# Performance work log

Measured on AMD Instinct MI355X. Metric: run time of the kernel, lower is better.

Reference implementation:

```python
import jax, jax.numpy as jnp
import numpy as np

RATIOS = (0.5, 1.0, 2.0)
SCALES = (8.0, 16.0, 32.0)
NUM_LANDMARKS = 6   # NMS max_output_size
IOU_THRESH = 0.5    # tf.image.non_max_suppression default


def _generate_anchors(fh, fw, ih, iw):
    # stride of backbone in each dim
    x_stride = iw / fw
    y_stride = ih / fh
    xs = (jnp.arange(fw, dtype=jnp.float32) + 0.5) * x_stride
    ys = (jnp.arange(fh, dtype=jnp.float32) + 0.5) * y_stride
    cy, cx = jnp.meshgrid(ys, xs, indexing='ij')              # [fh, fw]
    # 9 anchor (h, w) pairs: ratio-major, scale-minor
    h = jnp.array([np.sqrt(s * s / r) * y_stride for r in RATIOS for s in SCALES], jnp.float32)
    w = h * jnp.array([r for r in RATIOS for _ in SCALES], jnp.float32) * (x_stride / y_stride)
    cx = cx[..., None]
    cy = cy[..., None]
    anchors = jnp.stack([cx - w / 2, cy - h / 2, cx + w / 2, cy + h / 2], axis=-1)  # [fh,fw,9,4]
    anchors = anchors.reshape(-1, 4)                                               # [N,4]
    valid = (anchors[:, 0] >= 0) & (anchors[:, 1] >= 0) & \
            (anchors[:, 2] <= iw) & (anchors[:, 3] <= ih)
    return anchors, valid


def _conv(x, w, b):
    y = jax.lax.conv_general_dilated(x, w, (1, 1), 'SAME',
                                     dimension_numbers=('NHWC', 'HWIO', 'NHWC'))
    return y + b


def _iou_one_vs_all(box, boxes):
    x1 = jnp.maximum(box[0], boxes[:, 0])
    y1 = jnp.maximum(box[1], boxes[:, 1])
    x2 = jnp.minimum(box[2], boxes[:, 2])
    y2 = jnp.minimum(box[3], boxes[:, 3])
    inter = jnp.maximum(x2 - x1, 0.0) * jnp.maximum(y2 - y1, 0.0)
    a1 = (box[2] - box[0]) * (box[3] - box[1])
    a2 = (boxes[:, 2] - boxes[:, 0]) * (boxes[:, 3] - boxes[:, 1])
    return inter / (a1 + a2 - inter + 1e-9)


def setup_inputs() -> dict:
    key = jax.random.key(0)
    ks = jax.random.split(key, 8)
    STD = 0.05  # keras RandomNormal default stddev
    return {
        'features': jax.random.normal(ks[0], (1, 160, 160, 512), jnp.float32),
        'image':    jnp.zeros((1, 2560, 2560, 3), jnp.float32),  # only shape is consumed
        'conv1_w':  jax.random.normal(ks[1], (3, 3, 512, 512), jnp.float32) * STD,
        'conv1_b':  jnp.zeros((512,), jnp.float32),
        'reg_w':    jax.random.normal(ks[2], (1, 1, 512, 72), jnp.float32) * STD,
        'reg_b':    jnp.zeros((72,), jnp.float32),
        'cls_w':    jax.random.normal(ks[3], (1, 1, 512, 9), jnp.float32) * STD,
        'cls_b':    jnp.zeros((9,), jnp.float32),
        'lm_w':     jax.random.normal(ks[4], (1, 1, 512, 54), jnp.float32) * STD,
        'lm_b':     jnp.zeros((54,), jnp.float32),
    }


def reference(features, image, conv1_w, conv1_b, reg_w, reg_b, cls_w, cls_b, lm_w, lm_b):
    fh, fw = features.shape[1], features.shape[2]
    ih, iw = float(image.shape[1]), float(image.shape[2])
    anchors, valid = _generate_anchors(fh, fw, ih, iw)        # [N,4], [N]

    x = jax.nn.relu(_conv(features, conv1_w, conv1_b))        # [1,fh,fw,512]
    deltas = _conv(x, reg_w, reg_b).reshape(-1, 8)[:, :4]     # [N,4] (dx,dy,dw,dh)
    scores = jax.nn.sigmoid(_conv(x, cls_w, cls_b)).reshape(-1)  # [N]
    eye_landmarks = _conv(x, lm_w, lm_b)                      # [1,fh,fw,54]

    # decode anchor deltas -> corner boxes, clipped to the image
    wa = anchors[:, 2] - anchors[:, 0]
    ha = anchors[:, 3] - anchors[:, 1]
    xa = anchors[:, 0] + wa / 2
    ya = anchors[:, 1] + ha / 2
    px = xa + wa * deltas[:, 0]
    py = ya + ha * deltas[:, 1]
    pw = wa * jnp.exp(deltas[:, 2])
    ph = ha * jnp.exp(deltas[:, 3])
    x1 = px - pw / 2
    y1 = py - ph / 2
    boxes = jnp.stack([jnp.clip(x1, 0, iw), jnp.clip(y1, 0, ih),
                       jnp.clip(x1 + pw, 0, iw), jnp.clip(y1 + ph, 0, ih)], axis=-1)

    # greedy NMS, fixed 6 outputs (out-of-image anchors masked out)
    def body(k, carry):
        sel, alive = carry
        s = jnp.where(alive & valid, scores, -1.0)
        i = jnp.argmax(s).astype(jnp.int32)
        iou = _iou_one_vs_all(boxes[i], boxes)
        alive = alive & (iou <= IOU_THRESH)
        return sel.at[k].set(i), alive

    sel, _ = jax.lax.fori_loop(
        0, NUM_LANDMARKS, body,
        (jnp.zeros((NUM_LANDMARKS,), jnp.int32), jnp.ones((boxes.shape[0],), bool)))
    rois = boxes[sel]                                         # [6,4]
    return rois, eye_landmarks, anchors
```

## Files before the change

kernel.cpp:

```cpp
#include <hip/hip_runtime.h>
#include <math.h>

#define FH 160
#define FW 160
#define NPOS (FH*FW)
#define NANCH (NPOS*9)
#define IMG 2560.0f
#define STRIDE 16.0f

typedef __attribute__((ext_vector_type(8))) _Float16 half8;
typedef __attribute__((ext_vector_type(4))) float f32x4;
typedef unsigned long long u64;

__device__ __forceinline__ unsigned short f2h(float v) {
    _Float16 h = (_Float16)v;
    return *(unsigned short*)&h;
}
__device__ __forceinline__ void g2l16(void* lds, const void* g) {
    __builtin_amdgcn_global_load_lds(
        (const __attribute__((address_space(1))) void*)g,
        (__attribute__((address_space(3))) void*)lds, 16, 0, 0);
}
__device__ __forceinline__ u64 pack_key(float s, int n) {
    unsigned int bu = __float_as_uint(s);
    unsigned int key = (bu & 0x80000000u) ? ~bu : (bu | 0x80000000u);
    return ((u64)key << 32) | (unsigned int)~(unsigned int)n;
}
__device__ __forceinline__ u64 wave_max64(u64 v) {
#pragma unroll
    for (int off = 32; off > 0; off >>= 1) {
        u64 o = __shfl_xor(v, off, 64);
        v = v > o ? v : o;
    }
    return v;
}

__global__ __launch_bounds__(256) void prep_kernel(
    const float* __restrict__ f, const float* __restrict__ w,
    const float* __restrict__ regw, const float* __restrict__ clsw,
    const float* __restrict__ lmw,
    unsigned short* __restrict__ fph, unsigned short* __restrict__ wt,
    unsigned short* __restrict__ wh)
{
    __shared__ float tile[32][33];
    const int bid = blockIdx.x, t = threadIdx.x;
    if (bid < 13122) {
        int idx = bid*256 + t;
        int c4 = (idx & 127) << 2;
        int rest = idx >> 7;
        int x = rest % 162, y = rest / 162;
        float4 v = make_float4(0.f, 0.f, 0.f, 0.f);
        if (y > 0 && y < 161 && x > 0 && x < 161)
            v = *(const float4*)(f + ((size_t)((y-1)*FW + (x-1)) << 9) + c4);
        ushort4 h;
        h.x = f2h(v.x); h.y = f2h(v.y); h.z = f2h(v.z); h.w = f2h(v.w);
        *(ushort4*)(fph + ((size_t)(y*162 + x) << 9) + c4) = h;
    } else if (bid < 15426) {
        int b = bid - 13122;
        int k0 = (b % 144)*32, oc0 = (b / 144)*32;
        int c = t & 31, r8 = t >> 5;
#pragma unroll
        for (int i = 0; i < 4; ++i) {
            int r = r8 + i*8;
            tile[c][r] = w[(size_t)(k0 + r)*512 + oc0 + c];
        }
        __syncthreads();
#pragma unroll
        for (int i = 0; i < 4; ++i) {
            int orow = r8 + i*8, kcol = c;
            wt[(size_t)(oc0 + orow)*4608 + k0 + kcol] = f2h(tile[orow][kcol]);
        }
    } else {
        int i = (bid - 15426)*256 + t;
        int u = i >> 9, c = i & 511;
        float v = 0.f;
        if (u < 36)      v = regw[c*72 + (u>>2)*8 + (u&3)];
        else if (u < 45) v = clsw[c*9 + (u-36)];
        else if (u < 99) v = lmw[c*54 + (u-45)];
        wh[i] = f2h(v);
    }
}

__global__ __launch_bounds__(256) void conv1_mfma_kernel(
    const unsigned short* __restrict__ fph, const unsigned short* __restrict__ wt,
    const float* __restrict__ bias, unsigned short* __restrict__ xh)
{
    __shared__ unsigned short As[128*64];
    __shared__ unsigned short Bs[128*64];
    const int tid  = threadIdx.x;
    const int lane = tid & 63;
    const int wi   = (tid >> 7) & 1;
    const int wj   = (tid >> 6) & 1;
    const int bid  = blockIdx.x;
    const int xcd  = bid & 7, sl = bid >> 3;
    const int oc0  = (xcd & 3) * 128;
    const int pt   = (xcd >> 2) * 100 + sl;
    const int ty = pt / 5, tx = pt - ty*5;
    const int y0 = ty*4, x0 = tx*32;

    const int srow = tid >> 3;
    const int kswz = (((tid & 7) ^ (srow & 7)) << 3);
    const int quad = lane >> 4, fr = lane & 15;

    f32x4 acc[4][4] = {};
    const size_t bBase = (size_t)(oc0 + srow)*4608 + kswz;

    for (int tap = 0; tap < 9; ++tap) {
        const int ky = tap/3, kx = tap - (tap/3)*3;
        const size_t aBase = ((size_t)((y0 + ky)*162 + (x0 + srow + kx)) << 9) + kswz;
        const size_t bTap  = bBase + tap*512;
        for (int icb = 0; icb < 512; icb += 64) {
#pragma unroll
            for (int r = 0; r < 4; ++r) {
                g2l16(As + tid*8 + r*2048, fph + aBase + (size_t)r*162*512 + icb);
                g2l16(Bs + tid*8 + r*2048, wt  + bTap  + (size_t)r*32*4608 + icb);
            }
            __syncthreads();
#pragma unroll
            for (int kk = 0; kk < 2; ++kk) {
                const int sa = ((kk*4 + quad) ^ (fr & 7)) << 3;
                half8 a[4], b[4];
#pragma unroll
                for (int i = 0; i < 4; ++i) {
                    a[i] = *(const half8*)(As + (wi*64 + i*16 + fr)*64 + sa);
                    b[i] = *(const half8*)(Bs + (wj*64 + i*16 + fr)*64 + sa);
                }
#pragma unroll
                for (int i = 0; i < 4; ++i)
#pragma unroll
                    for (int j = 0; j < 4; ++j)
                        acc[i][j] = __builtin_amdgcn_mfma_f32_16x16x32_f16(a[i], b[j], acc[i][j], 0, 0, 0);
            }
            __syncthreads();
        }
    }

#pragma unroll
    for (int i = 0; i < 4; ++i) {
#pragma unroll
        for (int r = 0; r < 4; ++r) {
            int mi = wi*64 + i*16 + quad*4 + r;
            int p = (y0 + (mi >> 5))*FW + x0 + (mi & 31);
#pragma unroll
            for (int j = 0; j < 4; ++j) {
                int col = oc0 + wj*64 + j*16 + fr;
                float v = acc[i][j][r] + bias[col];
                xh[(size_t)p*512 + col] = f2h(v > 0.f ? v : 0.f);
            }
        }
    }
}

__global__ __launch_bounds__(256) void heads_mfma_kernel(
    const unsigned short* __restrict__ xh, const unsigned short* __restrict__ wh,
    const float* __restrict__ regb, const float* __restrict__ clsb,
    const float* __restrict__ lmb,
    float* __restrict__ lm_out, float* __restrict__ boxes,
    float* __restrict__ anch_out, float* __restrict__ s_arr,
    u64* __restrict__ blockmax)
{
    __shared__ union SM {
        struct { unsigned short As[128*64]; unsigned short Bs[128*64]; } g;
        struct { float sdel[128][40]; float scls[128][12]; u64 red[8]; } e;
    } sm;
    unsigned short* As = sm.g.As;
    unsigned short* Bs = sm.g.Bs;
    const int tid  = threadIdx.x;
    const int lane = tid & 63;
    const int wi   = (tid >> 7) & 1;
    const int wj   = (tid >> 6) & 1;
    const int p0   = blockIdx.x * 128;

    const int srow = tid >> 3;
    const int kswz = (((tid & 7) ^ (srow & 7)) << 3);
    const int quad = lane >> 4, fr = lane & 15;
    f32x4 acc[4][4] = {};

    const size_t aOfs = ((size_t)(p0 + srow) << 9) + kswz;
    const size_t bOfs = ((size_t)srow << 9) + kswz;

    for (int icb = 0; icb < 512; icb += 64) {
#pragma unroll
        for (int r = 0; r < 4; ++r) {
            g2l16(As + tid*8 + r*2048, xh + aOfs + (size_t)r*32*512 + icb);
            g2l16(Bs + tid*8 + r*2048, wh + bOfs + (size_t)r*32*512 + icb);
        }
        __syncthreads();
#pragma unroll
        for (int kk = 0; kk < 2; ++kk) {
            const int sa = ((kk*4 + quad) ^ (fr & 7)) << 3;
            half8 a[4], b[4];
#pragma unroll
            for (int i = 0; i < 4; ++i) {
                a[i] = *(const half8*)(As + (wi*64 + i*16 + fr)*64 + sa);
                b[i] = *(const half8*)(Bs + (wj*64 + i*16 + fr)*64 + sa);
            }
#pragma unroll
            for (int i = 0; i < 4; ++i)
#pragma unroll
                for (int j = 0; j < 4; ++j)
                    acc[i][j] = __builtin_amdgcn_mfma_f32_16x16x32_f16(a[i], b[j], acc[i][j], 0, 0, 0);
        }
        __syncthreads();
    }

#pragma unroll
    for (int i = 0; i < 4; ++i) {
#pragma unroll
        for (int r = 0; r < 4; ++r) {
            int pl = wi*64 + i*16 + quad*4 + r;
            int p = p0 + pl;
#pragma unroll
            for (int j = 0; j < 4; ++j) {
                int u = wj*64 + j*16 + fr;
                float v = acc[i][j][r];
                if (u < 36) {
                    sm.e.sdel[pl][u] = v + regb[(u>>2)*8 + (u&3)];
                } else if (u < 45) {
                    float z = v + clsb[u-36];
                    sm.e.scls[pl][u-36] = 1.f/(1.f + expf(-z));
                } else if (u < 99) {
                    lm_out[(size_t)p*54 + (u-45)] = v + lmb[u-45];
                }
            }
        }
    }
    __syncthreads();

    u64 local = 0ull;
    for (int t = tid; t < 128*9; t += 256) {
        int pl = t / 9, a = t - pl*9;
        int p = p0 + pl;
        int y = p / FW, x = p - FW*y;
        float cx = (x + 0.5f)*STRIDE, cy = (y + 0.5f)*STRIDE;
        const float rr[3] = {0.5f, 1.f, 2.f};
        const float ss[3] = {8.f, 16.f, 32.f};
        float r = rr[a/3], sv = ss[a - (a/3)*3];
        float h  = sqrtf(sv*sv/r)*STRIDE;
        float wvv = h * r;
        float x1a = cx - wvv*0.5f, y1a = cy - h*0.5f;
        float x2a = cx + wvv*0.5f, y2a = cy + h*0.5f;
        size_t n = (size_t)p*9 + a;
        float4 av = {x1a, y1a, x2a, y2a};
        *(float4*)(anch_out + 4*n) = av;
        bool valid = (x1a >= 0.f) && (y1a >= 0.f) && (x2a <= IMG) && (y2a <= IMG);

        float dx = sm.e.sdel[pl][a*4+0], dy = sm.e.sdel[pl][a*4+1];
        float dw = sm.e.sdel[pl][a*4+2], dh = sm.e.sdel[pl][a*4+3];
        float px = cx + wvv*dx, py = cy + h*dy;
        float pw = wvv*expf(dw), ph = h*expf(dh);
        float bx1 = px - pw*0.5f, by1 = py - ph*0.5f;
        float4 b;
        b.x = fminf(fmaxf(bx1, 0.f), IMG);
        b.y = fminf(fmaxf(by1, 0.f), IMG);
        b.z = fminf(fmaxf(bx1 + pw, 0.f), IMG);
        b.w = fminf(fmaxf(by1 + ph, 0.f), IMG);
        *(float4*)(boxes + 4*n) = b;
        float s = valid ? sm.e.scls[pl][a] : -1.f;
        s_arr[n] = s;
        u64 pk = pack_key(s, (int)n);
        local = local > pk ? local : pk;
    }
    local = wave_max64(local);
    if ((tid & 63) == 0) sm.e.red[tid >> 6] = local;
    __syncthreads();
    if (tid == 0) {
        u64 m = sm.e.red[0];
        m = m > sm.e.red[1] ? m : sm.e.red[1];
        m = m > sm.e.red[2] ? m : sm.e.red[2];
        m = m > sm.e.red[3] ? m : sm.e.red[3];
        blockmax[blockIdx.x] = m;
    }
}

__global__ __launch_bounds__(256) void nms_supp_kernel(
    const float* __restrict__ boxes, float* __restrict__ s_arr,
    u64* __restrict__ blockmax, float* __restrict__ rois, int k)
{
    __shared__ u64 red[4];
    __shared__ u64 win_sh;
    const int tid = threadIdx.x;

    u64 v = (tid < 200) ? blockmax[tid] : 0ull;
    v = wave_max64(v);
    if ((tid & 63) == 0) red[tid >> 6] = v;
    __syncthreads();
    if (tid == 0) {
        u64 m = red[0];
        m = m > red[1] ? m : red[1];
        m = m > red[2] ? m : red[2];
        m = m > red[3] ? m : red[3];
        win_sh = m;
    }
    __syncthreads();
    const unsigned int wn = ~(unsigned int)(win_sh & 0xFFFFFFFFull);
    const float4 wb = *(const float4*)(boxes + (size_t)4*wn);
    if (blockIdx.x == 0 && tid == 0)
        *(float4*)(rois + 4*(k-1)) = wb;

    const float wa = (wb.z - wb.x)*(wb.w - wb.y);
    const int base = blockIdx.x * 1152;
    u64 local = 0ull;
    for (int i = tid; i < 1152; i += 256) {
        int n = base + i;
        float s = s_arr[n];
        float4 b = *(const float4*)(boxes + (size_t)4*n);
        float ix = fminf(wb.z, b.z) - fmaxf(wb.x, b.x);
        float iy = fminf(wb.w, b.w) - fmaxf(wb.y, b.y);
        float inter = fmaxf(ix, 0.f)*fmaxf(iy, 0.f);
        float a2 = (b.z - b.x)*(b.w - b.y);
        float iou = inter/(wa + a2 - inter + 1e-9f);
        if (iou > 0.5f && s > -1.f) { s = -1.f; s_arr[n] = -1.f; }
        u64 pk = pack_key(s, n);
        local = local > pk ? local : pk;
    }
    local = wave_max64(local);
    if ((tid & 63) == 0) red[tid >> 6] = local;
    __syncthreads();
    if (tid == 0) {
        u64 m = red[0];
        m = m > red[1] ? m : red[1];
        m = m > red[2] ? m : red[2];
        m = m > red[3] ? m : red[3];
        blockmax[blockIdx.x] = m;
    }
}

__global__ void nms_fin2_kernel(
    const float* __restrict__ boxes, const u64* __restrict__ blockmax,
    float* __restrict__ rois)
{
    __shared__ u64 red[4];
    const int tid = threadIdx.x;
    u64 v = (tid < 200) ? blockmax[tid] : 0ull;
    v = wave_max64(v);
    if ((tid & 63) == 0) red[tid >> 6] = v;
    __syncthreads();
    if (tid == 0) {
        u64 m = red[0];
        m = m > red[1] ? m : red[1];
        m = m > red[2] ? m : red[2];
        m = m > red[3] ? m : red[3];
        unsigned int wn = ~(unsigned int)(m & 0xFFFFFFFFull);
        *(float4*)(rois + 20) = *(const float4*)(boxes + (size_t)4*wn);
    }
}

__global__ __launch_bounds__(256) void conv1_kernel(
    const float* __restrict__ f, const float* __restrict__ w,
    const float* __restrict__ bias, float* __restrict__ xout)
{
    __shared__ float As2[32][66];
    __shared__ float Bs2[32][66];
    const int tid = threadIdx.x;
    const int nt = blockIdx.x;
    const int mt = blockIdx.y;
    const int p0 = mt*64, oc0 = nt*64;
    const int tm = tid & 15, tn = tid >> 4;
    const int kA = tid & 31, mA = tid >> 5;
    const int nB = tid & 63, kB = tid >> 6;
    int yv[8], xv[8];
#pragma unroll
    for (int it = 0; it < 8; ++it) {
        int p = p0 + mA + it*8;
        yv[it] = p / FW;
        xv[it] = p - yv[it]*FW;
    }
    float acc[4][4] = {};
    for (int tap = 0; tap < 9; ++tap) {
        const int ky = tap/3 - 1, kx = tap%3 - 1;
        for (int icb = 0; icb < 512; icb += 32) {
#pragma unroll
            for (int it = 0; it < 8; ++it) {
                int yy = yv[it] + ky, xx = xv[it] + kx;
                float v = 0.f;
                if ((unsigned)yy < (unsigned)FH && (unsigned)xx < (unsigned)FW)
                    v = f[(((yy*FW)+xx)<<9) + icb + kA];
                As2[kA][mA + it*8] = v;
            }
            const float* wp = w + ((size_t)(tap*512 + icb + kB))*512 + oc0 + nB;
#pragma unroll
            for (int it = 0; it < 8; ++it)
                Bs2[kB + it*4][nB] = wp[(size_t)it*4*512];
            __syncthreads();
#pragma unroll 8
            for (int kk = 0; kk < 32; ++kk) {
                float a0 = As2[kk][4*tm+0], a1 = As2[kk][4*tm+1],
                      a2 = As2[kk][4*tm+2], a3 = As2[kk][4*tm+3];
                float b0 = Bs2[kk][4*tn+0], b1 = Bs2[kk][4*tn+1],
                      b2 = Bs2[kk][4*tn+2], b3 = Bs2[kk][4*tn+3];
                acc[0][0] += a0*b0; acc[0][1] += a0*b1; acc[0][2] += a0*b2; acc[0][3] += a0*b3;
                acc[1][0] += a1*b0; acc[1][1] += a1*b1; acc[1][2] += a1*b2; acc[1][3] += a1*b3;
                acc[2][0] += a2*b0; acc[2][1] += a2*b1; acc[2][2] += a2*b2; acc[2][3] += a2*b3;
                acc[3][0] += a3*b0; acc[3][1] += a3*b1; acc[3][2] += a3*b2; acc[3][3] += a3*b3;
            }
            __syncthreads();
        }
    }
#pragma unroll
    for (int i = 0; i < 4; ++i) {
        int p = p0 + 4*tm + i;
        float4 o;
        float* op = &o.x;
#pragma unroll
        for (int j = 0; j < 4; ++j) {
            float v = acc[i][j] + bias[oc0 + 4*tn + j];
            op[j] = v > 0.f ? v : 0.f;
        }
        *(float4*)(xout + (size_t)p*512 + oc0 + 4*tn) = o;
    }
}

__global__ __launch_bounds__(256) void wprep_kernel(
    const float* __restrict__ regw, const float* __restrict__ clsw,
    const float* __restrict__ lmw, float* __restrict__ wT)
{
    int i = blockIdx.x*256 + threadIdx.x;
    if (i >= 99*512) return;
    int u = i >> 9, c = i & 511;
    float v;
    if (u < 36)      v = regw[c*72 + (u>>2)*8 + (u&3)];
    else if (u < 45) v = clsw[c*9 + (u-36)];
    else             v = lmw[c*54 + (u-45)];
    wT[i] = v;
}

__global__ __launch_bounds__(256) void heads_kernel(
    const float* __restrict__ x, const float* __restrict__ wT,
    const float* __restrict__ regb, const float* __restrict__ clsb,
    const float* __restrict__ lmb,
    float* __restrict__ lm_out, float* __restrict__ deltas,
    float* __restrict__ s_arr)
{
    __shared__ float xs[16*516];
    const int p0 = blockIdx.x * 16;
    const float4* src = (const float4*)(x + (size_t)p0*512);
    for (int i = threadIdx.x; i < 16*128; i += 256) {
        int row = i >> 7, c4 = i & 127;
        *(float4*)(xs + row*516 + c4*4) = src[row*128 + c4];
    }
    __syncthreads();
    for (int oi = threadIdx.x; oi < 99*16; oi += 256) {
        int ps = oi & 15, u = oi >> 4;
        const float4* wv = (const float4*)(wT + (u << 9));
        const float4* xv = (const float4*)(xs + ps*516);
        float acc = 0.f;
#pragma unroll 4
        for (int c = 0; c < 128; ++c) {
            float4 a = xv[c], b = wv[c];
            acc += a.x*b.x + a.y*b.y + a.z*b.z + a.w*b.w;
        }
        int p = p0 + ps;
        if (u < 36) {
            int aidx = u >> 2, r = u & 3;
            deltas[(size_t)(p*9 + aidx)*4 + r] = acc + regb[aidx*8 + r];
        } else if (u < 45) {
            float z = acc + clsb[u-36];
            s_arr[p*9 + (u-36)] = 1.f/(1.f + expf(-z));
        } else {
            lm_out[(size_t)p*54 + (u-45)] = acc + lmb[u-45];
        }
    }
}

__global__ __launch_bounds__(256) void decode_kernel(
    const float* __restrict__ deltas, float* __restrict__ s_arr,
    float* __restrict__ boxes, float* __restrict__ anch_out,
    u64* __restrict__ slot)
{
    int n = blockIdx.x*256 + threadIdx.x;
    if (n < 8) slot[n] = 0ull;
    if (n >= NANCH) return;
    int p = n / 9, a = n - 9*p;
    int y = p / FW, x = p - FW*y;
    float cx = (x + 0.5f)*STRIDE, cy = (y + 0.5f)*STRIDE;
    const float rr[3] = {0.5f, 1.f, 2.f};
    const float ss[3] = {8.f, 16.f, 32.f};
    float r = rr[a/3], sv = ss[a - (a/3)*3];
    float h  = sqrtf(sv*sv/r)*STRIDE;
    float wv = h * r;
    float x1a = cx - wv*0.5f, y1a = cy - h*0.5f;
    float x2a = cx + wv*0.5f, y2a = cy + h*0.5f;
    float4 av = {x1a, y1a, x2a, y2a};
    *(float4*)(anch_out + (size_t)4*n) = av;
    bool valid = (x1a >= 0.f) && (y1a >= 0.f) && (x2a <= IMG) && (y2a <= IMG);

    float4 d = *(const float4*)(deltas + (size_t)4*n);
    float px = cx + wv*d.x, py = cy + h*d.y;
    float pw = wv*expf(d.z), ph = h*expf(d.w);
    float bx1 = px - pw*0.5f, by1 = py - ph*0.5f;
    float4 b;
    b.x = fminf(fmaxf(bx1, 0.f), IMG);
    b.y = fminf(fmaxf(by1, 0.f), IMG);
    b.z = fminf(fmaxf(bx1 + pw, 0.f), IMG);
    b.w = fminf(fmaxf(by1 + ph, 0.f), IMG);
    *(float4*)(boxes + (size_t)4*n) = b;
    if (!valid) s_arr[n] = -1.f;
}

__global__ __launch_bounds__(256) void nms_iter_kernel(
    const float* __restrict__ boxes, float* __restrict__ s_arr,
    u64* __restrict__ slot, int k)
{
    __shared__ u64 red[4];
    int n = blockIdx.x*256 + threadIdx.x;
    float s = s_arr[n];
    if (k > 0) {
        unsigned int wn = ~(unsigned int)(slot[k-1] & 0xFFFFFFFFull);
        float4 wb = *(const float4*)(boxes + (size_t)4*wn);
        float4 b  = *(const float4*)(boxes + (size_t)4*n);
        float ix = fminf(wb.z, b.z) - fmaxf(wb.x, b.x);
        float iy = fminf(wb.w, b.w) - fmaxf(wb.y, b.y);
        float inter = fmaxf(ix, 0.f)*fmaxf(iy, 0.f);
        float a1 = (wb.z-wb.x)*(wb.w-wb.y);
        float a2 = (b.z-b.x)*(b.w-b.y);
        float iou = inter/(a1 + a2 - inter + 1e-9f);
        if (iou > 0.5f) { s = -1.f; s_arr[n] = -1.f; }
    }
    u64 packed = pack_key(s, n);
    packed = wave_max64(packed);
    if ((threadIdx.x & 63) == 0) red[threadIdx.x >> 6] = packed;
    __syncthreads();
    if (threadIdx.x == 0) {
        u64 m = red[0];
        m = m > red[1] ? m : red[1];
        m = m > red[2] ? m : red[2];
        m = m > red[3] ? m : red[3];
        atomicMax(&slot[k], m);
    }
}

__global__ void nms_fin_kernel(
    const float* __restrict__ boxes,
    const u64* __restrict__ slot, float* __restrict__ rois)
{
    int t = threadIdx.x;
    if (t < 6) {
        unsigned int n = ~(unsigned int)(slot[t] & 0xFFFFFFFFull);
        float4 b = *(const float4*)(boxes + (size_t)4*n);
        *(float4*)(rois + 4*t) = b;
    }
}

extern "C" void kernel_launch(void* const* d_in, const int* in_sizes, int n_in,
                              void* d_out, int out_size, void* d_ws, size_t ws_size,
                              hipStream_t stream)
{
    const float* f    = (const float*)d_in[0];
    const float* c1w  = (const float*)d_in[2];
    const float* c1b  = (const float*)d_in[3];
    const float* regw = (const float*)d_in[4];
    const float* regb = (const float*)d_in[5];
    const float* clsw = (const float*)d_in[6];
    const float* clsb = (const float*)d_in[7];
    const float* lmw  = (const float*)d_in[8];
    const float* lmb  = (const float*)d_in[9];

    float* out      = (float*)d_out;
    float* rois     = out;
    float* lm_out   = out + 24;
    float* anch_out = out + 24 + (size_t)NPOS*54;

    char* ws = (char*)d_ws;

    if (ws_size >= 62547968ull) {
        u64* blockmax = (u64*)ws;
        unsigned short* wh  = (unsigned short*)(ws + 2048);
        unsigned short* fph = (unsigned short*)(ws + 133120);
        unsigned short* wt  = (unsigned short*)(ws + 27006976);
        unsigned short* xh  = (unsigned short*)(ws + 31725568);
        float* boxes  = (float*)(ws + 57939968);
        float* s_arr  = (float*)(ws + 61626368);

        prep_kernel<<<15682, 256, 0, stream>>>(f, c1w, regw, clsw, lmw,
                                               fph, wt, wh);
        conv1_mfma_kernel<<<800, 256, 0, stream>>>(fph, wt, c1b, xh);
        heads_mfma_kernel<<<200, 256, 0, stream>>>(xh, wh, regb, clsb, lmb,
                                                   lm_out, boxes, anch_out,
                                                   s_arr, blockmax);
        for (int k = 1; k <= 5; ++k)
            nms_supp_kernel<<<200, 256, 0, stream>>>(boxes, s_arr, blockmax,
                                                     rois, k);
        nms_fin2_kernel<<<1, 256, 0, stream>>>(boxes, blockmax, rois);
    } else {
        u64* slot = (u64*)ws;
        float* wT     = (float*)(ws + 256);
        float* boxes  = (float*)(ws + 256 + 202752);
        float* deltas = (float*)(ws + 256 + 202752 + 3686400);
        float* s_arr  = (float*)(ws + 256 + 202752 + 2*3686400);
        float* x      = (float*)(ws + 256 + 202752 + 2*3686400 + 921600);

        wprep_kernel<<<(99*512 + 255)/256, 256, 0, stream>>>(regw, clsw, lmw, wT);
        conv1_kernel<<<dim3(8, 400), 256, 0, stream>>>(f, c1w, c1b, x);
        heads_kernel<<<NPOS/16, 256, 0, stream>>>(x, wT, regb, clsb, lmb,
                                                  lm_out, deltas, s_arr);
        decode_kernel<<<NANCH/256, 256, 0, stream>>>(deltas, s_arr, boxes,
                                                     anch_out, slot);
        for (int k = 0; k < 6; ++k)
            nms_iter_kernel<<<NANCH/256, 256, 0, stream>>>(boxes, s_arr, slot, k);
        nms_fin_kernel<<<1, 64, 0, stream>>>(boxes, slot, rois);
    }
}
```

Measured before the change: 388.5 us.

## Fuse NMS iterations into heads kernel via grid-wide barrier

```diff
diff --git a/kernel.cpp b/kernel.cpp
--- a/kernel.cpp
+++ b/kernel.cpp
@@ -7,6 +7,7 @@
 #define NANCH (NPOS*9)
 #define IMG 2560.0f
 #define STRIDE 16.0f
+#define NBLK 400
 
 typedef __attribute__((ext_vector_type(8))) _Float16 half8;
 typedef __attribute__((ext_vector_type(4))) float f32x4;
@@ -33,6 +34,20 @@
         v = v > o ? v : o;
     }
     return v;
+}
+__device__ __forceinline__ void gbar(unsigned* cnt, int phase) {
+    __syncthreads();
+    if (threadIdx.x == 0) {
+        __threadfence();
+        __hip_atomic_fetch_add(cnt, 1u, __ATOMIC_RELAXED,
+                               __HIP_MEMORY_SCOPE_AGENT);
+        while (__hip_atomic_load(cnt, __ATOMIC_RELAXED,
+                                 __HIP_MEMORY_SCOPE_AGENT)
+               < (unsigned)(NBLK*phase))
+            __builtin_amdgcn_s_sleep(8);
+    }
+    __syncthreads();
+    __threadfence();
 }
 
 __global__ __launch_bounds__(256) void prep_kernel(
@@ -40,10 +55,11 @@
     const float* __restrict__ regw, const float* __restrict__ clsw,
     const float* __restrict__ lmw,
     unsigned short* __restrict__ fph, unsigned short* __restrict__ wt,
-    unsigned short* __restrict__ wh)
+    unsigned short* __restrict__ wh, unsigned* __restrict__ cnt)
 {
     __shared__ float tile[32][33];
     const int bid = blockIdx.x, t = threadIdx.x;
+    if (bid == 0 && t == 0) *cnt = 0u;
     if (bid < 13122) {
         int idx = bid*256 + t;
         int c4 = (idx & 127) << 2;
@@ -157,11 +173,12 @@
     const float* __restrict__ lmb,
     float* __restrict__ lm_out, float* __restrict__ boxes,
     float* __restrict__ anch_out, float* __restrict__ s_arr,
-    u64* __restrict__ blockmax)
+    u64* __restrict__ blockmax, unsigned* __restrict__ cnt,
+    float* __restrict__ rois)
 {
     __shared__ union SM {
-        struct { unsigned short As[128*64]; unsigned short Bs[128*64]; } g;
-        struct { float sdel[128][40]; float scls[128][12]; u64 red[8]; } e;
+        struct { unsigned short As[64*64]; unsigned short Bs[128*64]; } g;
+        struct { float sdel[64][40]; float scls[64][12]; u64 red[4]; } e;
     } sm;
     unsigned short* As = sm.g.As;
     unsigned short* Bs = sm.g.Bs;
@@ -169,34 +186,36 @@
     const int lane = tid & 63;
     const int wi   = (tid >> 7) & 1;
     const int wj   = (tid >> 6) & 1;
-    const int p0   = blockIdx.x * 128;
+    const int p0   = blockIdx.x * 64;
 
     const int srow = tid >> 3;
     const int kswz = (((tid & 7) ^ (srow & 7)) << 3);
     const int quad = lane >> 4, fr = lane & 15;
-    f32x4 acc[4][4] = {};
+    f32x4 acc[2][4] = {};
 
     const size_t aOfs = ((size_t)(p0 + srow) << 9) + kswz;
     const size_t bOfs = ((size_t)srow << 9) + kswz;
 
     for (int icb = 0; icb < 512; icb += 64) {
 #pragma unroll
-        for (int r = 0; r < 4; ++r) {
+        for (int r = 0; r < 2; ++r)
             g2l16(As + tid*8 + r*2048, xh + aOfs + (size_t)r*32*512 + icb);
+#pragma unroll
+        for (int r = 0; r < 4; ++r)
             g2l16(Bs + tid*8 + r*2048, wh + bOfs + (size_t)r*32*512 + icb);
-        }
         __syncthreads();
 #pragma unroll
         for (int kk = 0; kk < 2; ++kk) {
             const int sa = ((kk*4 + quad) ^ (fr & 7)) << 3;
-            half8 a[4], b[4];
-#pragma unroll
-            for (int i = 0; i < 4; ++i) {
-                a[i] = *(const half8*)(As + (wi*64 + i*16 + fr)*64 + sa);
-                b[i] = *(const half8*)(Bs + (wj*64 + i*16 + fr)*64 + sa);
-            }
-#pragma unroll
-            for (int i = 0; i < 4; ++i)
+            half8 a[2], b[4];
+#pragma unroll
+            for (int i = 0; i < 2; ++i)
+                a[i] = *(const half8*)(As + (wi*32 + i*16 + fr)*64 + sa);
+#pragma unroll
+            for (int j = 0; j < 4; ++j)
+                b[j] = *(const half8*)(Bs + (wj*64 + j*16 + fr)*64 + sa);
+#pragma unroll
+            for (int i = 0; i < 2; ++i)
 #pragma unroll
                 for (int j = 0; j < 4; ++j)
                     acc[i][j] = __builtin_amdgcn_mfma_f32_16x16x32_f16(a[i], b[j], acc[i][j], 0, 0, 0);
@@ -205,10 +224,10 @@
     }
 
 #pragma unroll
-    for (int i = 0; i < 4; ++i) {
+    for (int i = 0; i < 2; ++i) {
 #pragma unroll
         for (int r = 0; r < 4; ++r) {
-            int pl = wi*64 + i*16 + quad*4 + r;
+            int pl = wi*32 + i*16 + quad*4 + r;
             int p = p0 + pl;
 #pragma unroll
             for (int j = 0; j < 4; ++j) {
@@ -228,7 +247,7 @@
     __syncthreads();
 
     u64 local = 0ull;
-    for (int t = tid; t < 128*9; t += 256) {
+    for (int t = tid; t < 64*9; t += 256) {
         int pl = t / 9, a = t - pl*9;
         int p = p0 + pl;
         int y = p / FW, x = p - FW*y;
@@ -269,80 +288,59 @@
         m = m > sm.e.red[1] ? m : sm.e.red[1];
         m = m > sm.e.red[2] ? m : sm.e.red[2];
         m = m > sm.e.red[3] ? m : sm.e.red[3];
-        blockmax[blockIdx.x] = m;
-    }
-}
-
-__global__ __launch_bounds__(256) void nms_supp_kernel(
-    const float* __restrict__ boxes, float* __restrict__ s_arr,
-    u64* __restrict__ blockmax, float* __restrict__ rois, int k)
-{
-    __shared__ u64 red[4];
-    __shared__ u64 win_sh;
-    const int tid = threadIdx.x;
-
-    u64 v = (tid < 200) ? blockmax[tid] : 0ull;
-    v = wave_max64(v);
-    if ((tid & 63) == 0) red[tid >> 6] = v;
-    __syncthreads();
-    if (tid == 0) {
-        u64 m = red[0];
-        m = m > red[1] ? m : red[1];
-        m = m > red[2] ? m : red[2];
-        m = m > red[3] ? m : red[3];
-        win_sh = m;
-    }
-    __syncthreads();
-    const unsigned int wn = ~(unsigned int)(win_sh & 0xFFFFFFFFull);
-    const float4 wb = *(const float4*)(boxes + (size_t)4*wn);
-    if (blockIdx.x == 0 && tid == 0)
-        *(float4*)(rois + 4*(k-1)) = wb;
-
-    const float wa = (wb.z - wb.x)*(wb.w - wb.y);
-    const int base = blockIdx.x * 1152;
-    u64 local = 0ull;
-    for (int i = tid; i < 1152; i += 256) {
-        int n = base + i;
-        float s = s_arr[n];
-        float4 b = *(const float4*)(boxes + (size_t)4*n);
-        float ix = fminf(wb.z, b.z) - fmaxf(wb.x, b.x);
-        float iy = fminf(wb.w, b.w) - fmaxf(wb.y, b.y);
-        float inter = fmaxf(ix, 0.f)*fmaxf(iy, 0.f);
-        float a2 = (b.z - b.x)*(b.w - b.y);
-        float iou = inter/(wa + a2 - inter + 1e-9f);
-        if (iou > 0.5f && s > -1.f) { s = -1.f; s_arr[n] = -1.f; }
-        u64 pk = pack_key(s, n);
-        local = local > pk ? local : pk;
-    }
-    local = wave_max64(local);
-    if ((tid & 63) == 0) red[tid >> 6] = local;
-    __syncthreads();
-    if (tid == 0) {
-        u64 m = red[0];
-        m = m > red[1] ? m : red[1];
-        m = m > red[2] ? m : red[2];
-        m = m > red[3] ? m : red[3];
-        blockmax[blockIdx.x] = m;
-    }
-}
-
-__global__ void nms_fin2_kernel(
-    const float* __restrict__ boxes, const u64* __restrict__ blockmax,
-    float* __restrict__ rois)
-{
-    __shared__ u64 red[4];
-    const int tid = threadIdx.x;
-    u64 v = (tid < 200) ? blockmax[tid] : 0ull;
-    v = wave_max64(v);
-    if ((tid & 63) == 0) red[tid >> 6] = v;
-    __syncthreads();
-    if (tid == 0) {
-        u64 m = red[0];
-        m = m > red[1] ? m : red[1];
-        m = m > red[2] ? m : red[2];
-        m = m > red[3] ? m : red[3];
-        unsigned int wn = ~(unsigned int)(m & 0xFFFFFFFFull);
-        *(float4*)(rois + 20) = *(const float4*)(boxes + (size_t)4*wn);
+        __hip_atomic_store(&blockmax[blockIdx.x], m, __ATOMIC_RELAXED,
+                           __HIP_MEMORY_SCOPE_AGENT);
+    }
+
+    for (int k = 1; k <= 6; ++k) {
+        gbar(cnt, k);
+        u64 v = 0ull;
+        for (int i = tid; i < NBLK; i += 256) {
+            u64 x = __hip_atomic_load(&blockmax[i], __ATOMIC_RELAXED,
+                                      __HIP_MEMORY_SCOPE_AGENT);
+            v = v > x ? v : x;
+        }
+        v = wave_max64(v);
+        if ((tid & 63) == 0) sm.e.red[tid >> 6] = v;
+        __syncthreads();
+        u64 m = sm.e.red[0];
+        m = m > sm.e.red[1] ? m : sm.e.red[1];
+        m = m > sm.e.red[2] ? m : sm.e.red[2];
+        m = m > sm.e.red[3] ? m : sm.e.red[3];
+        unsigned wn = ~(unsigned)(m & 0xFFFFFFFFull);
+        if (blockIdx.x == 0 && tid == 0)
+            *(float4*)(rois + 4*(k-1)) = *(const float4*)(boxes + (size_t)4*wn);
+        if (k == 6) break;
+        __syncthreads();
+
+        float4 wb = *(const float4*)(boxes + (size_t)4*wn);
+        float wa = (wb.z - wb.x)*(wb.w - wb.y);
+        u64 loc = 0ull;
+        const int base = blockIdx.x * 576;
+        for (int i2 = tid; i2 < 576; i2 += 256) {
+            int n = base + i2;
+            float s = s_arr[n];
+            float4 b = *(const float4*)(boxes + (size_t)4*n);
+            float ix = fminf(wb.z, b.z) - fmaxf(wb.x, b.x);
+            float iy = fminf(wb.w, b.w) - fmaxf(wb.y, b.y);
+            float inter = fmaxf(ix, 0.f)*fmaxf(iy, 0.f);
+            float a2 = (b.z - b.x)*(b.w - b.y);
+            float iou = inter/(wa + a2 - inter + 1e-9f);
+            if (iou > 0.5f && s > -1.f) { s = -1.f; s_arr[n] = -1.f; }
+            u64 pk = pack_key(s, n);
+            loc = loc > pk ? loc : pk;
+        }
+        loc = wave_max64(loc);
+        if ((tid & 63) == 0) sm.e.red[tid >> 6] = loc;
+        __syncthreads();
+        if (tid == 0) {
+            u64 mm = sm.e.red[0];
+            mm = mm > sm.e.red[1] ? mm : sm.e.red[1];
+            mm = mm > sm.e.red[2] ? mm : sm.e.red[2];
+            mm = mm > sm.e.red[3] ? mm : sm.e.red[3];
+            __hip_atomic_store(&blockmax[blockIdx.x], mm, __ATOMIC_RELAXED,
+                               __HIP_MEMORY_SCOPE_AGENT);
+        }
     }
 }
 
@@ -563,25 +561,22 @@
 
     char* ws = (char*)d_ws;
 
-    if (ws_size >= 62547968ull) {
+    if (ws_size >= 62550016ull) {
         u64* blockmax = (u64*)ws;
-        unsigned short* wh  = (unsigned short*)(ws + 2048);
-        unsigned short* fph = (unsigned short*)(ws + 133120);
-        unsigned short* wt  = (unsigned short*)(ws + 27006976);
-        unsigned short* xh  = (unsigned short*)(ws + 31725568);
-        float* boxes  = (float*)(ws + 57939968);
-        float* s_arr  = (float*)(ws + 61626368);
+        unsigned* cnt = (unsigned*)(ws + 3584);
+        unsigned short* wh  = (unsigned short*)(ws + 4096);
+        unsigned short* fph = (unsigned short*)(ws + 135168);
+        unsigned short* wt  = (unsigned short*)(ws + 27009024);
+        unsigned short* xh  = (unsigned short*)(ws + 31727616);
+        float* boxes  = (float*)(ws + 57942016);
+        float* s_arr  = (float*)(ws + 61628416);
 
         prep_kernel<<<15682, 256, 0, stream>>>(f, c1w, regw, clsw, lmw,
-                                               fph, wt, wh);
+                                               fph, wt, wh, cnt);
         conv1_mfma_kernel<<<800, 256, 0, stream>>>(fph, wt, c1b, xh);
-        heads_mfma_kernel<<<200, 256, 0, stream>>>(xh, wh, regb, clsb, lmb,
-                                                   lm_out, boxes, anch_out,
-                                                   s_arr, blockmax);
-        for (int k = 1; k <= 5; ++k)
-            nms_supp_kernel<<<200, 256, 0, stream>>>(boxes, s_arr, blockmax,
-                                                     rois, k);
-        nms_fin2_kernel<<<1, 256, 0, stream>>>(boxes, blockmax, rois);
+        heads_mfma_kernel<<<NBLK, 256, 0, stream>>>(xh, wh, regb, clsb, lmb,
+                                                    lm_out, boxes, anch_out,
+                                                    s_arr, blockmax, cnt, rois);
     } else {
         u64* slot = (u64*)ws;
         float* wT     = (float*)(ws + 256);
```

Result: slower. 647.7 us (+66.7%).
